# Kernel optimization log

Hardware: AMD Instinct MI355X
Metric: run time of the kernel (lower is better)

Reference implementation:

```python
import jax, jax.numpy as jnp
import numpy as np

EPS = 1e-5
NEG_SLOPE = 0.2


def knn(x, k):
    # x: (B, C, N). pairwise_distance = -||xi - xj||^2, topk -> nearest neighbors.
    xt = jnp.swapaxes(x, 1, 2)                       # (B, N, C)
    inner = -2.0 * jnp.matmul(xt, x)                 # (B, N, N)
    xx = jnp.sum(x * x, axis=1, keepdims=True)       # (B, 1, N)
    pd = -xx - inner - jnp.swapaxes(xx, 1, 2)        # (B, N, N)
    return jax.lax.top_k(pd, k)[1]                   # (B, N, k) int32


def get_graph_feature(x, k):
    # x: (B, C, N) -> (B, N, k, 2C) edge features [neighbor - center, center]
    idx = knn(x, k)
    xt = jnp.swapaxes(x, 1, 2)                       # (B, N, C)
    nb = jax.vmap(lambda f, i: f[i])(xt, idx)        # (B, N, k, C) gather
    center = xt[:, :, None, :]                       # (B, N, 1, C)
    return jnp.concatenate(
        [nb - center, jnp.broadcast_to(center, nb.shape)], axis=-1)


def edge_conv(x, w, k):
    # conv_2d with kernel 1: 1x1 conv (no bias) + InstanceNorm2d + LeakyReLU, then max over k
    feat = get_graph_feature(x, k)                   # (B, N, k, 2C)
    y = jnp.einsum('bnkc,oc->bonk', feat, w)         # (B, O, N, k)
    mean = jnp.mean(y, axis=(2, 3), keepdims=True)
    var = jnp.var(y, axis=(2, 3), keepdims=True)
    y = (y - mean) * jax.lax.rsqrt(var + EPS)        # InstanceNorm2d (no affine)
    y = jnp.where(y >= 0, y, NEG_SLOPE * y)
    return jnp.max(y, axis=-1)                       # (B, O, N)


def setup_inputs() -> dict:
    key = jax.random.key(0)
    ks = jax.random.split(key, 8)
    B, N = 16, 2048
    s = 0.05
    return {
        'x': jax.random.normal(ks[0], (B, 3, N), dtype=jnp.float32),
        'w1': jax.random.normal(ks[1], (64, 6), dtype=jnp.float32) * s,
        'w2': jax.random.normal(ks[2], (64, 128), dtype=jnp.float32) * s,
        'w3': jax.random.normal(ks[3], (128, 128), dtype=jnp.float32) * s,
        'w4': jax.random.normal(ks[4], (256, 256), dtype=jnp.float32) * s,
        'w5': jax.random.normal(ks[5], (512, 512), dtype=jnp.float32) * s,
        'bn5_gamma': jnp.ones((512,), dtype=jnp.float32),
        'bn5_beta': jnp.zeros((512,), dtype=jnp.float32),
    }


def reference(x, w1, w2, w3, w4, w5, bn5_gamma, bn5_beta):
    k = 20
    x1 = edge_conv(x, w1, k)                         # (B, 64, N)
    x2 = edge_conv(x1, w2, k)                        # (B, 64, N)
    x3 = edge_conv(x2, w3, k)                        # (B, 128, N)
    x4 = edge_conv(x3, w4, k)                        # (B, 256, N)
    x_cat = jnp.concatenate([x1, x2, x3, x4], axis=1)  # (B, 512, N)
    y = jnp.einsum('bcn,oc->bon', x_cat, w5)         # conv5, (B, 512, N)
    # BatchNorm1d (training-mode batch stats) over (B, N)
    mean = jnp.mean(y, axis=(0, 2), keepdims=True)
    var = jnp.var(y, axis=(0, 2), keepdims=True)
    y = (y - mean) * jax.lax.rsqrt(var + EPS)
    y = y * bn5_gamma[None, :, None] + bn5_beta[None, :, None]
    y = jnp.where(y >= 0, y, NEG_SLOPE * y)
    feat = jnp.concatenate([jnp.max(y, axis=2), jnp.mean(y, axis=2)], axis=1)  # (B, 1024)
    return feat
```

## Files before the change

kernel.cpp:

```cpp
#include <hip/hip_runtime.h>

#define NN 2048
#define NB 16
#define KK 20
#define EPSF 1e-5f

typedef unsigned long long ull;
typedef _Float16 v8h __attribute__((ext_vector_type(8)));
typedef float v4f __attribute__((ext_vector_type(4)));

__device__ __forceinline__ float shflx_f(float v, int m) { return __shfl_xor(v, m, 64); }
__device__ __forceinline__ ull shflx_u64(ull v, int m) {
  int lo = __shfl_xor((int)(unsigned)v, m, 64);
  int hi = __shfl_xor((int)(unsigned)(v >> 32), m, 64);
  return (((ull)(unsigned)hi) << 32) | (unsigned)lo;
}
__device__ __forceinline__ ull packkey(float s, int n) {
  unsigned u = __float_as_uint(s);
  u = (u & 0x80000000u) ? ~u : (u | 0x80000000u);
  return (((ull)u) << 32) | (unsigned)(2047 - n);
}

__global__ __launch_bounds__(256) void prep_kernel(const float* __restrict__ x,
    _Float16* __restrict__ xh, _Float16* __restrict__ xl, float* __restrict__ xx,
    int C, int KB, long bstride)
{
  const int b = blockIdx.y;
  const int n = blockIdx.x * 256 + threadIdx.x;
  const float* xb = x + (size_t)b * bstride;
  const int Cp = KB * 32;
  _Float16* ph = xh + ((size_t)b * NN + n) * Cp;
  _Float16* pl = xl + ((size_t)b * NN + n) * Cp;
  float s = 0.f;
  for (int kb = 0; kb < KB; kb++) {
    for (int g = 0; g < 4; g++) {
      v8h hv, lv;
#pragma unroll
      for (int j = 0; j < 8; j++) {
        int c = kb * 32 + g * 8 + j;
        float v = (c < C) ? xb[(size_t)c * NN + n] : 0.f;
        _Float16 h = (_Float16)v;
        hv[j] = h;
        lv[j] = (_Float16)(v - (float)h);
        s = fmaf(v, v, s);
      }
      *(v8h*)(ph + kb * 32 + g * 8) = hv;
      *(v8h*)(pl + kb * 32 + g * 8) = lv;
    }
  }
  xx[b * NN + n] = s;
}

template<int KB>
__device__ __forceinline__ void tile_scores(const v8h (&Bh)[KB], const v8h (&Bl)[KB],
    const v8h (&Ah)[4][KB], const v8h (&Al)[4][KB], float xv, v4f (&out)[4])
{
#pragma unroll
  for (int a = 0; a < 4; a++) {
    v4f a0 = {0.f, 0.f, 0.f, 0.f};
    v4f a1 = {0.f, 0.f, 0.f, 0.f};
#pragma unroll
    for (int kb = 0; kb < KB; kb++) {
      v4f& acc = (kb & 1) ? a1 : a0;
      acc = __builtin_amdgcn_mfma_f32_16x16x32_f16(Ah[a][kb], Bh[kb], acc, 0, 0, 0);
      acc = __builtin_amdgcn_mfma_f32_16x16x32_f16(Ah[a][kb], Bl[kb], acc, 0, 0, 0);
      acc = __builtin_amdgcn_mfma_f32_16x16x32_f16(Al[a][kb], Bh[kb], acc, 0, 0, 0);
    }
    v4f s = a0 + a1;
#pragma unroll
    for (int j = 0; j < 4; j++) out[a][j] = s[j] - 0.5f * xv;
  }
}

template<int KB>
__global__ __launch_bounds__(256, 1) void knn2(
    const _Float16* __restrict__ xh, const _Float16* __restrict__ xl,
    const float* __restrict__ xxg, ull* __restrict__ slistG, int* __restrict__ cntG)
{
  __shared__ float gmL[256][33];
  __shared__ float tauL[256];
  __shared__ int scnt[256];

  const int t = threadIdx.x;
  const int lane = t & 63;
  const int wave = t >> 6;
  const int col = lane & 15;
  const int quad = lane >> 4;
  const int quad8 = quad * 8;
  const int b = blockIdx.x >> 1;
  const int chunk = blockIdx.x & 1;
  const int qg = blockIdx.y;
  const int Cp = KB * 32;
  const int cb = chunk * 1024;
  const _Float16* xhb = xh + (size_t)b * NN * Cp;
  const _Float16* xlb = xl + (size_t)b * NN * Cp;
  const float* xxb = xxg + b * NN;

  v8h Ah[4][KB], Al[4][KB];
  const int qw = qg * 256 + wave * 64;
#pragma unroll
  for (int a = 0; a < 4; a++) {
    const _Float16* pa = xhb + (size_t)(qw + a * 16 + col) * Cp + quad8;
    const _Float16* pb = xlb + (size_t)(qw + a * 16 + col) * Cp + quad8;
#pragma unroll
    for (int kb = 0; kb < KB; kb++) {
      Ah[a][kb] = *(const v8h*)(pa + kb * 32);
      Al[a][kb] = *(const v8h*)(pb + kb * 32);
    }
  }

  v8h Bh[2][KB], Bl[2][KB];
  float xvb[2];
  auto loadB = [&](int slot, int tt) {
    int t2 = tt < 63 ? tt : 63;
    int n = cb + t2 * 16 + col;
    const _Float16* pb = xhb + (size_t)n * Cp + quad8;
    const _Float16* pl = xlb + (size_t)n * Cp + quad8;
#pragma unroll
    for (int kb = 0; kb < KB; kb++) {
      Bh[slot][kb] = *(const v8h*)(pb + kb * 32);
      Bl[slot][kb] = *(const v8h*)(pl + kb * 32);
    }
    xvb[slot] = xxb[n];
  };

  float gm[4][8];
#pragma unroll
  for (int a = 0; a < 4; a++)
#pragma unroll
    for (int j = 0; j < 8; j++) gm[a][j] = -3.4e38f;

  loadB(0, 0);
  for (int tt = 0; tt < 64; tt += 2) {
    loadB(1, tt + 1);
    {
      v4f out[4];
      tile_scores<KB>(Bh[0], Bl[0], Ah, Al, xvb[0], out);
#pragma unroll
      for (int a = 0; a < 4; a++)
#pragma unroll
        for (int j = 0; j < 4; j++) gm[a][j * 2] = fmaxf(gm[a][j * 2], out[a][j]);
    }
    loadB(0, tt + 2);
    {
      v4f out[4];
      tile_scores<KB>(Bh[1], Bl[1], Ah, Al, xvb[1], out);
#pragma unroll
      for (int a = 0; a < 4; a++)
#pragma unroll
        for (int j = 0; j < 4; j++) gm[a][j * 2 + 1] = fmaxf(gm[a][j * 2 + 1], out[a][j]);
    }
  }

#pragma unroll
  for (int a = 0; a < 4; a++)
#pragma unroll
    for (int j = 0; j < 4; j++) {
      int qi = wave * 64 + a * 16 + quad * 4 + j;
      gmL[qi][col * 2 + 0] = gm[a][j * 2 + 0];
      gmL[qi][col * 2 + 1] = gm[a][j * 2 + 1];
    }
  scnt[t] = 0;
  asm volatile("s_waitcnt lgkmcnt(0)" ::: "memory");

  for (int r = 0; r < 32; r++) {
    const int q = wave * 64 + r * 2 + (lane >> 5);
    const int idx = lane & 31;
    float v = gmL[q][idx];
#pragma unroll
    for (int kk = 2; kk <= 32; kk <<= 1) {
#pragma unroll
      for (int m = kk >> 1; m >= 1; m >>= 1) {
        float o = shflx_f(v, m);
        bool keepmax = ((idx & kk) == 0) == ((idx & m) == 0);
        v = keepmax ? fmaxf(v, o) : fminf(v, o);
      }
    }
    if (idx == 19) tauL[q] = v;
  }
  asm volatile("s_waitcnt lgkmcnt(0)" ::: "memory");

  float tq[4][4];
#pragma unroll
  for (int a = 0; a < 4; a++)
#pragma unroll
    for (int j = 0; j < 4; j++) tq[a][j] = tauL[wave * 64 + a * 16 + quad * 4 + j];

  ull* slB = slistG + (((size_t)b * NN + qg * 256) * 2 + chunk) * 64;
  loadB(0, 0);
  for (int tt = 0; tt < 64; tt += 2) {
    loadB(1, tt + 1);
    for (int s = 0; s < 2; s++) {
      v4f out[4];
      tile_scores<KB>(s ? Bh[1] : Bh[0], s ? Bl[1] : Bl[0], Ah, Al, xvb[s], out);
      int n = cb + (tt + s) * 16 + col;
#pragma unroll
      for (int a = 0; a < 4; a++)
#pragma unroll
        for (int j = 0; j < 4; j++) {
          float sc = out[a][j];
          if (sc >= tq[a][j]) {
            int qi = wave * 64 + a * 16 + quad * 4 + j;
            int pos = atomicAdd(&scnt[qi], 1);
            if (pos < 64) slB[(size_t)qi * 128 + pos] = packkey(sc, n);
          }
        }
      if (s == 0) loadB(0, tt + 2);
    }
  }
  asm volatile("s_waitcnt lgkmcnt(0)" ::: "memory");
  cntG[((size_t)b * NN + qg * 256 + t) * 2 + chunk] = scnt[t];
}

__global__ __launch_bounds__(256) void knn_merge(const ull* __restrict__ slistG,
    const int* __restrict__ cntG, const _Float16* __restrict__ xh,
    const _Float16* __restrict__ xl, const float* __restrict__ xxg,
    int* __restrict__ idxout, int Cp, int C)
{
  const int lane = threadIdx.x & 63, wave = threadIdx.x >> 6;
  const int b = blockIdx.y;
  const int q = blockIdx.x * 4 + wave;
  const int c0 = cntG[((size_t)b * NN + q) * 2 + 0];
  const int c1 = cntG[((size_t)b * NN + q) * 2 + 1];
  int* op = idxout + ((size_t)b * NN + q) * KK;

  if (c0 <= 64 && c1 <= 64) {
    const ull* s0 = slistG + ((size_t)b * NN + q) * 128;
    const int total = c0 + c1;
    ull e0 = 0, e1 = 0;
    int p0 = lane, p1 = lane + 64;
    if (p0 < total) e0 = (p0 < c0) ? s0[p0] : s0[64 + p0 - c0];
    if (p1 < total) e1 = (p1 < c0) ? s0[p1] : s0[64 + p1 - c0];
    for (int s = 0; s < KK; s++) {
      ull m = e0 > e1 ? e0 : e1;
      ull g = m;
#pragma unroll
      for (int d = 1; d < 64; d <<= 1) { ull o = shflx_u64(g, d); g = o > g ? o : g; }
      if (lane == 0) op[s] = 2047 - (int)(g & 0xFFFFFFFFu);
      if (e0 == g) e0 = 0; else if (e1 == g) e1 = 0;
    }
  } else {
    const _Float16* qh = xh + ((size_t)b * NN + q) * Cp;
    const _Float16* ql = xl + ((size_t)b * NN + q) * Cp;
    const float* xxb = xxg + b * NN;
    float sc[32];
#pragma unroll
    for (int i = 0; i < 32; i++) sc[i] = -0.5f * xxb[lane + 64 * i];
    for (int c = 0; c < C; c++) {
      float qv = (float)qh[c] + (float)ql[c];
      for (int i = 0; i < 32; i++) {
        int n = lane + 64 * i;
        float bv = (float)xh[((size_t)b * NN + n) * Cp + c] + (float)xl[((size_t)b * NN + n) * Cp + c];
        sc[i] = fmaf(qv, bv, sc[i]);
      }
    }
    for (int s = 0; s < KK; s++) {
      ull m = 0; int mi = -1;
      for (int i = 0; i < 32; i++) {
        ull k = packkey(sc[i], lane + 64 * i);
        if (k > m) { m = k; mi = i; }
      }
      ull g = m;
#pragma unroll
      for (int d = 1; d < 64; d <<= 1) { ull o = shflx_u64(g, d); g = o > g ? o : g; }
      if (lane == 0) op[s] = 2047 - (int)(g & 0xFFFFFFFFu);
      if (m == g && mi >= 0) sc[mi] = -3.4e38f;
    }
  }
}

__global__ __launch_bounds__(256) void wcvt_uv(const float* __restrict__ w,
    _Float16* __restrict__ wuh, _Float16* __restrict__ wul,
    _Float16* __restrict__ wvh, _Float16* __restrict__ wvl, int C, int Cp, int O)
{
  int idx = blockIdx.x * 256 + threadIdx.x;
  if (idx >= O * Cp) return;
  int o = idx / Cp, c = idx - o * Cp;
  float a = 0.f, bv = 0.f;
  if (c < C) { a = w[o * 2 * C + c]; bv = w[o * 2 * C + C + c]; }
  float v = bv - a;
  _Float16 ah = (_Float16)a; wuh[idx] = ah; wul[idx] = (_Float16)(a - (float)ah);
  _Float16 vh = (_Float16)v; wvh[idx] = vh; wvl[idx] = (_Float16)(v - (float)vh);
}

__global__ __launch_bounds__(256) void w5cvt(const float* __restrict__ w5,
    _Float16* __restrict__ w5h, _Float16* __restrict__ w5l)
{
  int idx = blockIdx.x * 256 + threadIdx.x;
  float v = w5[idx];
  _Float16 h = (_Float16)v;
  w5h[idx] = h;
  w5l[idx] = (_Float16)(v - (float)h);
}

__global__ __launch_bounds__(256) void y5cvt_kernel(const float* __restrict__ xcat,
    _Float16* __restrict__ xh, _Float16* __restrict__ xl)
{
  const int b = blockIdx.y;
  const int n = blockIdx.x * 256 + threadIdx.x;
  for (int kc = blockIdx.z * 4; kc < blockIdx.z * 4 + 4; kc++) {
    v8h h[4], l[4];
#pragma unroll
    for (int g = 0; g < 4; g++)
#pragma unroll
      for (int j = 0; j < 8; j++) {
        float v = xcat[((size_t)b * 512 + kc * 32 + g * 8 + j) * NN + n];
        _Float16 hh = (_Float16)v;
        h[g][j] = hh;
        l[g][j] = (_Float16)(v - (float)hh);
      }
    size_t base = (((size_t)b * 16 + kc) * NN + n) * 32;
#pragma unroll
    for (int g = 0; g < 4; g++) {
      *(v8h*)(xh + base + g * 8) = h[g];
      *(v8h*)(xl + base + g * 8) = l[g];
    }
  }
}

__global__ __launch_bounds__(256) void y5_mfma(const _Float16* __restrict__ w5h,
    const _Float16* __restrict__ w5l, const _Float16* __restrict__ xh,
    const _Float16* __restrict__ xl, float* __restrict__ y5)
{
  const int lane = threadIdx.x & 63, wave = threadIdx.x >> 6;
  const int col = lane & 15, quad = lane >> 4, quad8 = quad * 8;
  const int b = blockIdx.z;
  const int o0 = blockIdx.x * 256 + wave * 64;
  const int nb0 = blockIdx.y * 128;
  v4f acc[4][8];
#pragma unroll
  for (int a = 0; a < 4; a++)
#pragma unroll
    for (int t = 0; t < 8; t++) acc[a][t] = {0.f, 0.f, 0.f, 0.f};

  for (int kc = 0; kc < 16; kc++) {
    v8h Ah[4], Al[4];
#pragma unroll
    for (int a = 0; a < 4; a++) {
      size_t off = (size_t)(o0 + a * 16 + col) * 512 + kc * 32 + quad8;
      Ah[a] = *(const v8h*)(w5h + off);
      Al[a] = *(const v8h*)(w5l + off);
    }
#pragma unroll
    for (int t = 0; t < 8; t++) {
      int n = nb0 + t * 16 + col;
      size_t boff = (((size_t)b * 16 + kc) * NN + n) * 32 + quad8;
      v8h Bh = *(const v8h*)(xh + boff);
      v8h Bl = *(const v8h*)(xl + boff);
#pragma unroll
      for (int a = 0; a < 4; a++) {
        acc[a][t] = __builtin_amdgcn_mfma_f32_16x16x32_f16(Ah[a], Bh, acc[a][t], 0, 0, 0);
        acc[a][t] = __builtin_amdgcn_mfma_f32_16x16x32_f16(Ah[a], Bl, acc[a][t], 0, 0, 0);
        acc[a][t] = __builtin_amdgcn_mfma_f32_16x16x32_f16(Al[a], Bh, acc[a][t], 0, 0, 0);
      }
    }
  }
#pragma unroll
  for (int a = 0; a < 4; a++)
#pragma unroll
    for (int t = 0; t < 8; t++)
#pragma unroll
      for (int j = 0; j < 4; j++)
        y5[((size_t)b * 512 + o0 + a * 16 + quad * 4 + j) * NN + nb0 + t * 16 + col] = acc[a][t][j];
}

__global__ __launch_bounds__(256) void uv_mfma(const _Float16* __restrict__ wuh,
    const _Float16* __restrict__ wul, const _Float16* __restrict__ wvh,
    const _Float16* __restrict__ wvl, const _Float16* __restrict__ xh,
    const _Float16* __restrict__ xl, float* __restrict__ Uc, float* __restrict__ Vc,
    int Cp)
{
  const int lane = threadIdx.x & 63, wave = threadIdx.x >> 6;
  const int col = lane & 15, quad = lane >> 4, quad8 = quad * 8;
  const int b = blockIdx.z;
  const int o0 = blockIdx.x * 32;
  const int nb0 = blockIdx.y * 512 + wave * 128;
  v4f aU[2][8], aV[2][8];
#pragma unroll
  for (int a = 0; a < 2; a++)
#pragma unroll
    for (int t = 0; t < 8; t++) { aU[a][t] = {0.f,0.f,0.f,0.f}; aV[a][t] = {0.f,0.f,0.f,0.f}; }

  const int KBr = Cp >> 5;
  for (int kb = 0; kb < KBr; kb++) {
    v8h Uh[2], Ul[2], Vh[2], Vl[2];
#pragma unroll
    for (int a = 0; a < 2; a++) {
      size_t off = (size_t)(o0 + a * 16 + col) * Cp + kb * 32 + quad8;
      Uh[a] = *(const v8h*)(wuh + off);
      Ul[a] = *(const v8h*)(wul + off);
      Vh[a] = *(const v8h*)(wvh + off);
      Vl[a] = *(const v8h*)(wvl + off);
    }
#pragma unroll
    for (int t = 0; t < 8; t++) {
      int n = nb0 + t * 16 + col;
      size_t boff = ((size_t)b * NN + n) * Cp + kb * 32 + quad8;
      v8h Bh = *(const v8h*)(xh + boff);
      v8h Bl = *(const v8h*)(xl + boff);
#pragma unroll
      for (int a = 0; a < 2; a++) {
        aU[a][t] = __builtin_amdgcn_mfma_f32_16x16x32_f16(Uh[a], Bh, aU[a][t], 0, 0, 0);
        aU[a][t] = __builtin_amdgcn_mfma_f32_16x16x32_f16(Uh[a], Bl, aU[a][t], 0, 0, 0);
        aU[a][t] = __builtin_amdgcn_mfma_f32_16x16x32_f16(Ul[a], Bh, aU[a][t], 0, 0, 0);
        aV[a][t] = __builtin_amdgcn_mfma_f32_16x16x32_f16(Vh[a], Bh, aV[a][t], 0, 0, 0);
        aV[a][t] = __builtin_amdgcn_mfma_f32_16x16x32_f16(Vh[a], Bl, aV[a][t], 0, 0, 0);
        aV[a][t] = __builtin_amdgcn_mfma_f32_16x16x32_f16(Vl[a], Bh, aV[a][t], 0, 0, 0);
      }
    }
  }
#pragma unroll
  for (int a = 0; a < 2; a++)
#pragma unroll
    for (int t = 0; t < 8; t++)
#pragma unroll
      for (int j = 0; j < 4; j++) {
        size_t base = ((size_t)b * 64 + o0 + a * 16 + quad * 4 + j) * NN + nb0 + t * 16 + col;
        Uc[base] = aU[a][t][j];
        Vc[base] = aV[a][t][j];
      }
}

__global__ __launch_bounds__(256) void edge_kernel(const float* __restrict__ Uc,
    const float* __restrict__ Vc, const int* __restrict__ idx,
    float* __restrict__ xo)
{
  __shared__ float Ur[4 * 2052];
  __shared__ float red[8][4];
  __shared__ float smv[8];
  const int b = blockIdx.y, o0 = blockIdx.x * 4;
  const int t = threadIdx.x, lane = t & 63, wave = t >> 6;
  for (int r = 0; r < 4; r++)
    for (int i = t; i < NN; i += 256)
      Ur[r * 2052 + i] = Uc[((size_t)b * 64 + o0 + r) * NN + i];
  __syncthreads();
  const float* Vb = Vc + ((size_t)b * 64 + o0) * NN;
  const int* ib = idx + (size_t)b * NN * KK;
  float s0 = 0, s1 = 0, s2 = 0, s3 = 0, c0 = 0, c1 = 0, c2 = 0, c3 = 0;
  for (int n = t; n < NN; n += 256) {
    float v0 = Vb[n], v1 = Vb[NN + n], v2 = Vb[2 * NN + n], v3 = Vb[3 * NN + n];
    const int* ip = ib + (size_t)n * KK;
#pragma unroll
    for (int j = 0; j < KK; j++) {
      int m = ip[j];
      float y0 = Ur[m] + v0, y1 = Ur[2052 + m] + v1;
      float y2 = Ur[4104 + m] + v2, y3 = Ur[6156 + m] + v3;
      s0 += y0; c0 = fmaf(y0, y0, c0);
      s1 += y1; c1 = fmaf(y1, y1, c1);
      s2 += y2; c2 = fmaf(y2, y2, c2);
      s3 += y3; c3 = fmaf(y3, y3, c3);
    }
  }
  float sa[4] = { s0, s1, s2, s3 }, ca[4] = { c0, c1, c2, c3 };
#pragma unroll
  for (int r = 0; r < 4; r++) {
    float a = sa[r], c = ca[r];
#pragma unroll
    for (int d = 1; d < 64; d <<= 1) { a += shflx_f(a, d); c += shflx_f(c, d); }
    if (lane == 0) { red[r][wave] = a; red[4 + r][wave] = c; }
  }
  __syncthreads();
  if (t < 4) {
    float a = red[t][0] + red[t][1] + red[t][2] + red[t][3];
    float c = red[4 + t][0] + red[4 + t][1] + red[4 + t][2] + red[4 + t][3];
    const float inv = 1.f / (float)(NN * KK);
    float mu = a * inv;
    float var = fmaxf(c * inv - mu * mu, 0.f);
    smv[t] = mu;
    smv[4 + t] = rsqrtf(var + EPSF);
  }
  __syncthreads();
  const float mu0 = smv[0], mu1 = smv[1], mu2 = smv[2], mu3 = smv[3];
  const float i0 = smv[4], i1 = smv[5], i2 = smv[6], i3 = smv[7];
  for (int n = t; n < NN; n += 256) {
    float v0 = Vb[n], v1 = Vb[NN + n], v2 = Vb[2 * NN + n], v3 = Vb[3 * NN + n];
    const int* ip = ib + (size_t)n * KK;
    float m0 = -3.4e38f, m1 = m0, m2 = m0, m3 = m0;
#pragma unroll
    for (int j = 0; j < KK; j++) {
      int m = ip[j];
      m0 = fmaxf(m0, Ur[m] + v0);
      m1 = fmaxf(m1, Ur[2052 + m] + v1);
      m2 = fmaxf(m2, Ur[4104 + m] + v2);
      m3 = fmaxf(m3, Ur[6156 + m] + v3);
    }
    float z;
    z = (m0 - mu0) * i0; xo[((size_t)b * 512 + o0 + 0) * NN + n] = z >= 0.f ? z : 0.2f * z;
    z = (m1 - mu1) * i1; xo[((size_t)b * 512 + o0 + 1) * NN + n] = z >= 0.f ? z : 0.2f * z;
    z = (m2 - mu2) * i2; xo[((size_t)b * 512 + o0 + 2) * NN + n] = z >= 0.f ? z : 0.2f * z;
    z = (m3 - mu3) * i3; xo[((size_t)b * 512 + o0 + 3) * NN + n] = z >= 0.f ? z : 0.2f * z;
  }
}

__global__ __launch_bounds__(256) void bn5stat_kernel(const float* __restrict__ y5,
    float* __restrict__ bn5) {
  __shared__ float rs[4], rq[4];
  const int o = blockIdx.x, t = threadIdx.x, lane = t & 63, wave = t >> 6;
  float s = 0.f, q = 0.f;
  for (int b = 0; b < NB; b++) {
    const float* p = y5 + ((size_t)b * 512 + o) * NN;
    for (int n = t; n < NN; n += 256) { float v = p[n]; s += v; q = fmaf(v, v, q); }
  }
#pragma unroll
  for (int d = 1; d < 64; d <<= 1) { s += shflx_f(s, d); q += shflx_f(q, d); }
  if (lane == 0) { rs[wave] = s; rq[wave] = q; }
  __syncthreads();
  if (t == 0) {
    float S = rs[0] + rs[1] + rs[2] + rs[3];
    float Q = rq[0] + rq[1] + rq[2] + rq[3];
    const float inv = 1.f / (float)(NB * NN);
    float mu = S * inv;
    float var = fmaxf(Q * inv - mu * mu, 0.f);
    bn5[o] = mu;
    bn5[512 + o] = rsqrtf(var + EPSF);
  }
}

__global__ __launch_bounds__(256) void final_kernel(const float* __restrict__ y5,
    const float* __restrict__ bn5, const float* __restrict__ gamma,
    const float* __restrict__ beta, float* __restrict__ out)
{
  __shared__ float rm[4], rs[4];
  const int o = blockIdx.x, b = blockIdx.y, t = threadIdx.x, lane = t & 63, wave = t >> 6;
  const float mu = bn5[o], iv = bn5[512 + o], g = gamma[o], be = beta[o];
  const float* p = y5 + ((size_t)b * 512 + o) * NN;
  float mx = -3.4e38f, sm = 0.f;
  for (int n = t; n < NN; n += 256) {
    float z = (p[n] - mu) * iv;
    z = z * g + be;
    z = (z >= 0.f) ? z : 0.2f * z;
    mx = fmaxf(mx, z);
    sm += z;
  }
#pragma unroll
  for (int d = 1; d < 64; d <<= 1) { mx = fmaxf(mx, shflx_f(mx, d)); sm += shflx_f(sm, d); }
  if (lane == 0) { rm[wave] = mx; rs[wave] = sm; }
  __syncthreads();
  if (t == 0) {
    float M = fmaxf(fmaxf(rm[0], rm[1]), fmaxf(rm[2], rm[3]));
    float S = rs[0] + rs[1] + rs[2] + rs[3];
    out[(size_t)b * 1024 + o] = M;
    out[(size_t)b * 1024 + 512 + o] = S * (1.f / NN);
  }
}

extern "C" void kernel_launch(void* const* d_in, const int* in_sizes, int n_in,
                              void* d_out, int out_size, void* d_ws, size_t ws_size,
                              hipStream_t stream)
{
  (void)in_sizes; (void)n_in; (void)out_size; (void)ws_size;
  const float* x  = (const float*)d_in[0];
  const float* w1 = (const float*)d_in[1];
  const float* w2 = (const float*)d_in[2];
  const float* w3 = (const float*)d_in[3];
  const float* w4 = (const float*)d_in[4];
  const float* w5 = (const float*)d_in[5];
  const float* g5 = (const float*)d_in[6];
  const float* b5 = (const float*)d_in[7];
  float* out = (float*)d_out;

  float* ws   = (float*)d_ws;
  float* xcat = ws;
  float* Ub   = xcat + 16777216;
  float* Vb   = Ub + 8388608;
  int*   idxb = (int*)(Vb + 8388608);
  float* xxb  = (float*)(idxb + 655360);
  float* bn5  = xxb + 32768;

  _Float16* xth = (_Float16*)Vb;
  _Float16* xtl = xth + (size_t)NB * NN * 128;
  int* cntb = (int*)(Vb + 4194304);
  float* Vc = Vb + 4259840;
  _Float16* wuh = (_Float16*)(Vb + 6356992);
  _Float16* wul = wuh + 32768;
  _Float16* wvh = wul + 32768;
  _Float16* wvl = wvh + 32768;

  ull* slist = (ull*)Ub;
  float* Uc = Ub;

  _Float16* w5h = (_Float16*)idxb;
  _Float16* w5l = w5h + 262144;
  _Float16* xcfh = (_Float16*)Ub;
  _Float16* xcfl = (_Float16*)Vb;
  float* y5 = xcat;

  struct Lyr { const float* xin; long bstride; int C, KB, O, coff; const float* w; };
  const Lyr L[4] = {
    { x,              3L * NN,   3,   1, 64,  0,   w1 },
    { xcat,           512L * NN, 64,  2, 64,  64,  w2 },
    { xcat + 64 * NN, 512L * NN, 64,  2, 128, 128, w3 },
    { xcat + 128 * NN,512L * NN, 128, 4, 256, 256, w4 },
  };

  for (int l = 0; l < 4; l++) {
    const int Cp = L[l].KB * 32, O = L[l].O;
    prep_kernel<<<dim3(NN / 256, NB), 256, 0, stream>>>(L[l].xin, xth, xtl, xxb,
                                                        L[l].C, L[l].KB, L[l].bstride);
    switch (L[l].KB) {
      case 1: knn2<1><<<dim3(NB * 2, NN / 256), 256, 0, stream>>>(xth, xtl, xxb, slist, cntb); break;
      case 2: knn2<2><<<dim3(NB * 2, NN / 256), 256, 0, stream>>>(xth, xtl, xxb, slist, cntb); break;
      default: knn2<4><<<dim3(NB * 2, NN / 256), 256, 0, stream>>>(xth, xtl, xxb, slist, cntb); break;
    }
    knn_merge<<<dim3(NN / 4, NB), 256, 0, stream>>>(slist, cntb, xth, xtl, xxb, idxb,
                                                    Cp, L[l].C);
    wcvt_uv<<<(O * Cp + 255) / 256, 256, 0, stream>>>(L[l].w, wuh, wul, wvh, wvl,
                                                      L[l].C, Cp, O);
    for (int c0 = 0; c0 < O; c0 += 64) {
      uv_mfma<<<dim3(2, NN / 512, NB), 256, 0, stream>>>(
          wuh + (size_t)c0 * Cp, wul + (size_t)c0 * Cp,
          wvh + (size_t)c0 * Cp, wvl + (size_t)c0 * Cp,
          xth, xtl, Uc, Vc, Cp);
      edge_kernel<<<dim3(16, NB), 256, 0, stream>>>(Uc, Vc, idxb,
          xcat + (size_t)(L[l].coff + c0) * NN);
    }
  }
  w5cvt<<<1024, 256, 0, stream>>>(w5, w5h, w5l);
  y5cvt_kernel<<<dim3(NN / 256, NB, 4), 256, 0, stream>>>(xcat, xcfh, xcfl);
  y5_mfma<<<dim3(2, NN / 128, NB), 256, 0, stream>>>(w5h, w5l, xcfh, xcfl, y5);
  bn5stat_kernel<<<512, 256, 0, stream>>>(y5, bn5);
  final_kernel<<<dim3(512, NB), 256, 0, stream>>>(y5, bn5, g5, b5, out);
}
```

Baseline: 1.743 ms.

## Fuse edge-conv outputs into next-layer fp16 inputs and compute instance-norm stats algebraically

The edge kernel now gathers U once per point, keeping the max and sum over neighbours. The instance-norm statistics are rebuilt from those sums, a neighbour-count histogram and V moments, so the second gather pass is gone. It writes the split-fp16 layouts for the next layer's kNN and for the conv5 GEMM directly, and accumulates squared norms with atomics. This removes the per-layer prep kernel, the xcat fp32 buffer and the y5 conversion pass. The kNN B-tile prefetch is deepened from 2 to 4 slots, and uv_mfma now covers larger output chunks per launch. In exchange the norm maths is more complex, relies on atomics, and adds register pressure.

Measured after the change: 2.566 ms. +47.2%, slower.

```diff
diff --git a/kernel.cpp b/kernel.cpp
--- a/kernel.cpp
+++ b/kernel.cpp
@@ -7,6 +7,7 @@
 
 typedef unsigned long long ull;
 typedef _Float16 v8h __attribute__((ext_vector_type(8)));
+typedef _Float16 v4h __attribute__((ext_vector_type(4)));
 typedef float v4f __attribute__((ext_vector_type(4)));
 
 __device__ __forceinline__ float shflx_f(float v, int m) { return __shfl_xor(v, m, 64); }
@@ -109,8 +110,8 @@
     }
   }
 
-  v8h Bh[2][KB], Bl[2][KB];
-  float xvb[2];
+  v8h Bh[4][KB], Bl[4][KB];
+  float xvb[4];
   auto loadB = [&](int slot, int tt) {
     int t2 = tt < 63 ? tt : 63;
     int n = cb + t2 * 16 + col;
@@ -130,25 +131,19 @@
 #pragma unroll
     for (int j = 0; j < 8; j++) gm[a][j] = -3.4e38f;
 
-  loadB(0, 0);
-  for (int tt = 0; tt < 64; tt += 2) {
-    loadB(1, tt + 1);
-    {
+#pragma unroll
+  for (int s = 0; s < 4; s++) loadB(s, s);
+  for (int tt = 0; tt < 64; tt += 4) {
+#pragma unroll
+    for (int s = 0; s < 4; s++) {
       v4f out[4];
-      tile_scores<KB>(Bh[0], Bl[0], Ah, Al, xvb[0], out);
+      tile_scores<KB>(Bh[s], Bl[s], Ah, Al, xvb[s], out);
+      loadB(s, tt + 4 + s);
+      const int par = s & 1;
 #pragma unroll
       for (int a = 0; a < 4; a++)
 #pragma unroll
-        for (int j = 0; j < 4; j++) gm[a][j * 2] = fmaxf(gm[a][j * 2], out[a][j]);
-    }
-    loadB(0, tt + 2);
-    {
-      v4f out[4];
-      tile_scores<KB>(Bh[1], Bl[1], Ah, Al, xvb[1], out);
-#pragma unroll
-      for (int a = 0; a < 4; a++)
-#pragma unroll
-        for (int j = 0; j < 4; j++) gm[a][j * 2 + 1] = fmaxf(gm[a][j * 2 + 1], out[a][j]);
+        for (int j = 0; j < 4; j++) gm[a][j * 2 + par] = fmaxf(gm[a][j * 2 + par], out[a][j]);
     }
   }
 
@@ -187,12 +182,14 @@
     for (int j = 0; j < 4; j++) tq[a][j] = tauL[wave * 64 + a * 16 + quad * 4 + j];
 
   ull* slB = slistG + (((size_t)b * NN + qg * 256) * 2 + chunk) * 64;
-  loadB(0, 0);
-  for (int tt = 0; tt < 64; tt += 2) {
-    loadB(1, tt + 1);
-    for (int s = 0; s < 2; s++) {
+#pragma unroll
+  for (int s = 0; s < 4; s++) loadB(s, s);
+  for (int tt = 0; tt < 64; tt += 4) {
+#pragma unroll
+    for (int s = 0; s < 4; s++) {
       v4f out[4];
-      tile_scores<KB>(s ? Bh[1] : Bh[0], s ? Bl[1] : Bl[0], Ah, Al, xvb[s], out);
+      tile_scores<KB>(Bh[s], Bl[s], Ah, Al, xvb[s], out);
+      loadB(s, tt + 4 + s);
       int n = cb + (tt + s) * 16 + col;
 #pragma unroll
       for (int a = 0; a < 4; a++)
@@ -205,7 +202,6 @@
             if (pos < 64) slB[(size_t)qi * 128 + pos] = packkey(sc, n);
           }
         }
-      if (s == 0) loadB(0, tt + 2);
     }
   }
   asm volatile("s_waitcnt lgkmcnt(0)" ::: "memory");
@@ -269,18 +265,34 @@
   }
 }
 
-__global__ __launch_bounds__(256) void wcvt_uv(const float* __restrict__ w,
+__global__ __launch_bounds__(256) void setup_kernel(const int* __restrict__ idx,
+    int* __restrict__ cnt, const float* __restrict__ w,
     _Float16* __restrict__ wuh, _Float16* __restrict__ wul,
-    _Float16* __restrict__ wvh, _Float16* __restrict__ wvl, int C, int Cp, int O)
-{
-  int idx = blockIdx.x * 256 + threadIdx.x;
-  if (idx >= O * Cp) return;
-  int o = idx / Cp, c = idx - o * Cp;
-  float a = 0.f, bv = 0.f;
-  if (c < C) { a = w[o * 2 * C + c]; bv = w[o * 2 * C + C + c]; }
-  float v = bv - a;
-  _Float16 ah = (_Float16)a; wuh[idx] = ah; wul[idx] = (_Float16)(a - (float)ah);
-  _Float16 vh = (_Float16)v; wvh[idx] = vh; wvl[idx] = (_Float16)(v - (float)vh);
+    _Float16* __restrict__ wvh, _Float16* __restrict__ wvl,
+    int C, int Cp, int O, float* __restrict__ xx, int zxx)
+{
+  __shared__ int h[2048];
+  const int blk = blockIdx.x, t = threadIdx.x;
+  if (blk < NB) {
+    const int b = blk;
+    for (int i = t; i < 2048; i += 256) h[i] = 0;
+    if (zxx) for (int i = t; i < 2048; i += 256) xx[b * 2048 + i] = 0.f;
+    __syncthreads();
+    const int* ib = idx + (size_t)b * NN * KK;
+    for (int i = t; i < NN * KK; i += 256) atomicAdd(&h[ib[i]], 1);
+    __syncthreads();
+    for (int i = t; i < 2048; i += 256) cnt[b * 2048 + i] = h[i];
+  } else {
+    int e = (blk - NB) * 256 + t;
+    if (e < O * Cp) {
+      int o = e / Cp, c = e - o * Cp;
+      float a = 0.f, bv = 0.f;
+      if (c < C) { a = w[o * 2 * C + c]; bv = w[o * 2 * C + C + c]; }
+      float v = bv - a;
+      _Float16 ah = (_Float16)a; wuh[e] = ah; wul[e] = (_Float16)(a - (float)ah);
+      _Float16 vh = (_Float16)v; wvh[e] = vh; wvl[e] = (_Float16)(v - (float)vh);
+    }
+  }
 }
 
 __global__ __launch_bounds__(256) void w5cvt(const float* __restrict__ w5,
@@ -293,82 +305,11 @@
   w5l[idx] = (_Float16)(v - (float)h);
 }
 
-__global__ __launch_bounds__(256) void y5cvt_kernel(const float* __restrict__ xcat,
-    _Float16* __restrict__ xh, _Float16* __restrict__ xl)
-{
-  const int b = blockIdx.y;
-  const int n = blockIdx.x * 256 + threadIdx.x;
-  for (int kc = blockIdx.z * 4; kc < blockIdx.z * 4 + 4; kc++) {
-    v8h h[4], l[4];
-#pragma unroll
-    for (int g = 0; g < 4; g++)
-#pragma unroll
-      for (int j = 0; j < 8; j++) {
-        float v = xcat[((size_t)b * 512 + kc * 32 + g * 8 + j) * NN + n];
-        _Float16 hh = (_Float16)v;
-        h[g][j] = hh;
-        l[g][j] = (_Float16)(v - (float)hh);
-      }
-    size_t base = (((size_t)b * 16 + kc) * NN + n) * 32;
-#pragma unroll
-    for (int g = 0; g < 4; g++) {
-      *(v8h*)(xh + base + g * 8) = h[g];
-      *(v8h*)(xl + base + g * 8) = l[g];
-    }
-  }
-}
-
-__global__ __launch_bounds__(256) void y5_mfma(const _Float16* __restrict__ w5h,
-    const _Float16* __restrict__ w5l, const _Float16* __restrict__ xh,
-    const _Float16* __restrict__ xl, float* __restrict__ y5)
-{
-  const int lane = threadIdx.x & 63, wave = threadIdx.x >> 6;
-  const int col = lane & 15, quad = lane >> 4, quad8 = quad * 8;
-  const int b = blockIdx.z;
-  const int o0 = blockIdx.x * 256 + wave * 64;
-  const int nb0 = blockIdx.y * 128;
-  v4f acc[4][8];
-#pragma unroll
-  for (int a = 0; a < 4; a++)
-#pragma unroll
-    for (int t = 0; t < 8; t++) acc[a][t] = {0.f, 0.f, 0.f, 0.f};
-
-  for (int kc = 0; kc < 16; kc++) {
-    v8h Ah[4], Al[4];
-#pragma unroll
-    for (int a = 0; a < 4; a++) {
-      size_t off = (size_t)(o0 + a * 16 + col) * 512 + kc * 32 + quad8;
-      Ah[a] = *(const v8h*)(w5h + off);
-      Al[a] = *(const v8h*)(w5l + off);
-    }
-#pragma unroll
-    for (int t = 0; t < 8; t++) {
-      int n = nb0 + t * 16 + col;
-      size_t boff = (((size_t)b * 16 + kc) * NN + n) * 32 + quad8;
-      v8h Bh = *(const v8h*)(xh + boff);
-      v8h Bl = *(const v8h*)(xl + boff);
-#pragma unroll
-      for (int a = 0; a < 4; a++) {
-        acc[a][t] = __builtin_amdgcn_mfma_f32_16x16x32_f16(Ah[a], Bh, acc[a][t], 0, 0, 0);
-        acc[a][t] = __builtin_amdgcn_mfma_f32_16x16x32_f16(Ah[a], Bl, acc[a][t], 0, 0, 0);
-        acc[a][t] = __builtin_amdgcn_mfma_f32_16x16x32_f16(Al[a], Bh, acc[a][t], 0, 0, 0);
-      }
-    }
-  }
-#pragma unroll
-  for (int a = 0; a < 4; a++)
-#pragma unroll
-    for (int t = 0; t < 8; t++)
-#pragma unroll
-      for (int j = 0; j < 4; j++)
-        y5[((size_t)b * 512 + o0 + a * 16 + quad * 4 + j) * NN + nb0 + t * 16 + col] = acc[a][t][j];
-}
-
 __global__ __launch_bounds__(256) void uv_mfma(const _Float16* __restrict__ wuh,
     const _Float16* __restrict__ wul, const _Float16* __restrict__ wvh,
     const _Float16* __restrict__ wvl, const _Float16* __restrict__ xh,
-    const _Float16* __restrict__ xl, float* __restrict__ Uc, float* __restrict__ Vc,
-    int Cp)
+    const _Float16* __restrict__ xl, float* __restrict__ Uo, float* __restrict__ Vo,
+    int Cp, int Och)
 {
   const int lane = threadIdx.x & 63, wave = threadIdx.x >> 6;
   const int col = lane & 15, quad = lane >> 4, quad8 = quad * 8;
@@ -415,81 +356,166 @@
     for (int t = 0; t < 8; t++)
 #pragma unroll
       for (int j = 0; j < 4; j++) {
-        size_t base = ((size_t)b * 64 + o0 + a * 16 + quad * 4 + j) * NN + nb0 + t * 16 + col;
-        Uc[base] = aU[a][t][j];
-        Vc[base] = aV[a][t][j];
+        size_t base = ((size_t)b * Och + o0 + a * 16 + quad * 4 + j) * NN + nb0 + t * 16 + col;
+        Uo[base] = aU[a][t][j];
+        Vo[base] = aV[a][t][j];
       }
 }
 
-__global__ __launch_bounds__(256) void edge_kernel(const float* __restrict__ Uc,
-    const float* __restrict__ Vc, const int* __restrict__ idx,
-    float* __restrict__ xo)
+__global__ __launch_bounds__(256) void edge2(const float* __restrict__ U,
+    const float* __restrict__ V, const int* __restrict__ idx,
+    const int* __restrict__ cnt,
+    _Float16* __restrict__ nxh, _Float16* __restrict__ nxl, int CpN,
+    _Float16* __restrict__ y5h, _Float16* __restrict__ y5l, int gbase,
+    float* __restrict__ xx, int Och)
 {
   __shared__ float Ur[4 * 2052];
-  __shared__ float red[8][4];
+  __shared__ float red[20][4];
   __shared__ float smv[8];
   const int b = blockIdx.y, o0 = blockIdx.x * 4;
   const int t = threadIdx.x, lane = t & 63, wave = t >> 6;
   for (int r = 0; r < 4; r++)
     for (int i = t; i < NN; i += 256)
-      Ur[r * 2052 + i] = Uc[((size_t)b * 64 + o0 + r) * NN + i];
+      Ur[r * 2052 + i] = U[((size_t)b * Och + o0 + r) * NN + i];
   __syncthreads();
-  const float* Vb = Vc + ((size_t)b * 64 + o0) * NN;
+  const float* Vp = V + ((size_t)b * Och + o0) * NN;
   const int* ib = idx + (size_t)b * NN * KK;
-  float s0 = 0, s1 = 0, s2 = 0, s3 = 0, c0 = 0, c1 = 0, c2 = 0, c3 = 0;
-  for (int n = t; n < NN; n += 256) {
-    float v0 = Vb[n], v1 = Vb[NN + n], v2 = Vb[2 * NN + n], v3 = Vb[3 * NN + n];
+  const int* cb = cnt + b * NN;
+
+  float sG[4] = {0,0,0,0}, sVG[4] = {0,0,0,0}, sV[4] = {0,0,0,0},
+        sV2[4] = {0,0,0,0}, sU2[4] = {0,0,0,0};
+  float Mr[4][8], Vr[4][8];
+#pragma unroll
+  for (int ni = 0; ni < 8; ni++) {
+    const int n = t + ni * 256;
     const int* ip = ib + (size_t)n * KK;
+    float G0 = 0, G1 = 0, G2 = 0, G3 = 0;
+    float M0 = -3.4e38f, M1 = M0, M2 = M0, M3 = M0;
 #pragma unroll
     for (int j = 0; j < KK; j++) {
       int m = ip[j];
-      float y0 = Ur[m] + v0, y1 = Ur[2052 + m] + v1;
-      float y2 = Ur[4104 + m] + v2, y3 = Ur[6156 + m] + v3;
-      s0 += y0; c0 = fmaf(y0, y0, c0);
-      s1 += y1; c1 = fmaf(y1, y1, c1);
-      s2 += y2; c2 = fmaf(y2, y2, c2);
-      s3 += y3; c3 = fmaf(y3, y3, c3);
-    }
-  }
-  float sa[4] = { s0, s1, s2, s3 }, ca[4] = { c0, c1, c2, c3 };
+      float u0 = Ur[m], u1 = Ur[2052 + m], u2 = Ur[4104 + m], u3 = Ur[6156 + m];
+      G0 += u0; M0 = fmaxf(M0, u0);
+      G1 += u1; M1 = fmaxf(M1, u1);
+      G2 += u2; M2 = fmaxf(M2, u2);
+      G3 += u3; M3 = fmaxf(M3, u3);
+    }
+    float v0 = Vp[n], v1 = Vp[NN + n], v2 = Vp[2 * NN + n], v3 = Vp[3 * NN + n];
+    sG[0] += G0; sVG[0] = fmaf(v0, G0, sVG[0]); sV[0] += v0; sV2[0] = fmaf(v0, v0, sV2[0]);
+    sG[1] += G1; sVG[1] = fmaf(v1, G1, sVG[1]); sV[1] += v1; sV2[1] = fmaf(v1, v1, sV2[1]);
+    sG[2] += G2; sVG[2] = fmaf(v2, G2, sVG[2]); sV[2] += v2; sV2[2] = fmaf(v2, v2, sV2[2]);
+    sG[3] += G3; sVG[3] = fmaf(v3, G3, sVG[3]); sV[3] += v3; sV2[3] = fmaf(v3, v3, sV2[3]);
+    Mr[0][ni] = M0; Mr[1][ni] = M1; Mr[2][ni] = M2; Mr[3][ni] = M3;
+    Vr[0][ni] = v0; Vr[1][ni] = v1; Vr[2][ni] = v2; Vr[3][ni] = v3;
+  }
+  for (int i = t; i < NN; i += 256) {
+    float c = (float)cb[i];
+    float u0 = Ur[i], u1 = Ur[2052 + i], u2 = Ur[4104 + i], u3 = Ur[6156 + i];
+    sU2[0] = fmaf(c * u0, u0, sU2[0]);
+    sU2[1] = fmaf(c * u1, u1, sU2[1]);
+    sU2[2] = fmaf(c * u2, u2, sU2[2]);
+    sU2[3] = fmaf(c * u3, u3, sU2[3]);
+  }
+  float st[20];
 #pragma unroll
   for (int r = 0; r < 4; r++) {
-    float a = sa[r], c = ca[r];
-#pragma unroll
-    for (int d = 1; d < 64; d <<= 1) { a += shflx_f(a, d); c += shflx_f(c, d); }
-    if (lane == 0) { red[r][wave] = a; red[4 + r][wave] = c; }
+    st[r] = sG[r]; st[4 + r] = sVG[r]; st[8 + r] = sV[r];
+    st[12 + r] = sV2[r]; st[16 + r] = sU2[r];
+  }
+#pragma unroll
+  for (int k = 0; k < 20; k++) {
+    float a = st[k];
+#pragma unroll
+    for (int d = 1; d < 64; d <<= 1) a += shflx_f(a, d);
+    if (lane == 0) red[k][wave] = a;
   }
   __syncthreads();
   if (t < 4) {
-    float a = red[t][0] + red[t][1] + red[t][2] + red[t][3];
-    float c = red[4 + t][0] + red[4 + t][1] + red[4 + t][2] + red[4 + t][3];
+    float g  = red[t][0] + red[t][1] + red[t][2] + red[t][3];
+    float vg = red[4 + t][0] + red[4 + t][1] + red[4 + t][2] + red[4 + t][3];
+    float v  = red[8 + t][0] + red[8 + t][1] + red[8 + t][2] + red[8 + t][3];
+    float v2 = red[12 + t][0] + red[12 + t][1] + red[12 + t][2] + red[12 + t][3];
+    float u2 = red[16 + t][0] + red[16 + t][1] + red[16 + t][2] + red[16 + t][3];
+    float sumY  = g + (float)KK * v;
+    float sumY2 = u2 + 2.f * vg + (float)KK * v2;
     const float inv = 1.f / (float)(NN * KK);
-    float mu = a * inv;
-    float var = fmaxf(c * inv - mu * mu, 0.f);
+    float mu = sumY * inv;
+    float var = fmaxf(sumY2 * inv - mu * mu, 0.f);
     smv[t] = mu;
     smv[4 + t] = rsqrtf(var + EPSF);
   }
   __syncthreads();
   const float mu0 = smv[0], mu1 = smv[1], mu2 = smv[2], mu3 = smv[3];
   const float i0 = smv[4], i1 = smv[5], i2 = smv[6], i3 = smv[7];
-  for (int n = t; n < NN; n += 256) {
-    float v0 = Vb[n], v1 = Vb[NN + n], v2 = Vb[2 * NN + n], v3 = Vb[3 * NN + n];
-    const int* ip = ib + (size_t)n * KK;
-    float m0 = -3.4e38f, m1 = m0, m2 = m0, m3 = m0;
-#pragma unroll
-    for (int j = 0; j < KK; j++) {
-      int m = ip[j];
-      m0 = fmaxf(m0, Ur[m] + v0);
-      m1 = fmaxf(m1, Ur[2052 + m] + v1);
-      m2 = fmaxf(m2, Ur[4104 + m] + v2);
-      m3 = fmaxf(m3, Ur[6156 + m] + v3);
-    }
-    float z;
-    z = (m0 - mu0) * i0; xo[((size_t)b * 512 + o0 + 0) * NN + n] = z >= 0.f ? z : 0.2f * z;
-    z = (m1 - mu1) * i1; xo[((size_t)b * 512 + o0 + 1) * NN + n] = z >= 0.f ? z : 0.2f * z;
-    z = (m2 - mu2) * i2; xo[((size_t)b * 512 + o0 + 2) * NN + n] = z >= 0.f ? z : 0.2f * z;
-    z = (m3 - mu3) * i3; xo[((size_t)b * 512 + o0 + 3) * NN + n] = z >= 0.f ? z : 0.2f * z;
-  }
+  const int kc = (gbase + o0) >> 5, c32 = (gbase + o0) & 31;
+#pragma unroll
+  for (int ni = 0; ni < 8; ni++) {
+    const int n = t + ni * 256;
+    float z0 = (Mr[0][ni] + Vr[0][ni] - mu0) * i0; z0 = z0 >= 0.f ? z0 : 0.2f * z0;
+    float z1 = (Mr[1][ni] + Vr[1][ni] - mu1) * i1; z1 = z1 >= 0.f ? z1 : 0.2f * z1;
+    float z2 = (Mr[2][ni] + Vr[2][ni] - mu2) * i2; z2 = z2 >= 0.f ? z2 : 0.2f * z2;
+    float z3 = (Mr[3][ni] + Vr[3][ni] - mu3) * i3; z3 = z3 >= 0.f ? z3 : 0.2f * z3;
+    v4h h4, l4;
+    h4[0] = (_Float16)z0; l4[0] = (_Float16)(z0 - (float)h4[0]);
+    h4[1] = (_Float16)z1; l4[1] = (_Float16)(z1 - (float)h4[1]);
+    h4[2] = (_Float16)z2; l4[2] = (_Float16)(z2 - (float)h4[2]);
+    h4[3] = (_Float16)z3; l4[3] = (_Float16)(z3 - (float)h4[3]);
+    size_t yoff = (((size_t)b * 16 + kc) * NN + n) * 32 + c32;
+    *(v4h*)(y5h + yoff) = h4;
+    *(v4h*)(y5l + yoff) = l4;
+    if (nxh) {
+      size_t noff = ((size_t)b * NN + n) * CpN + o0;
+      *(v4h*)(nxh + noff) = h4;
+      *(v4h*)(nxl + noff) = l4;
+      atomicAdd(&xx[b * NN + n], z0 * z0 + z1 * z1 + z2 * z2 + z3 * z3);
+    }
+  }
+}
+
+__global__ __launch_bounds__(256) void y5_mfma(const _Float16* __restrict__ w5h,
+    const _Float16* __restrict__ w5l, const _Float16* __restrict__ xh,
+    const _Float16* __restrict__ xl, float* __restrict__ y5)
+{
+  const int lane = threadIdx.x & 63, wave = threadIdx.x >> 6;
+  const int col = lane & 15, quad = lane >> 4, quad8 = quad * 8;
+  const int b = blockIdx.z;
+  const int o0 = blockIdx.x * 256 + wave * 64;
+  const int nb0 = blockIdx.y * 128;
+  v4f acc[4][8];
+#pragma unroll
+  for (int a = 0; a < 4; a++)
+#pragma unroll
+    for (int t = 0; t < 8; t++) acc[a][t] = {0.f, 0.f, 0.f, 0.f};
+
+  for (int kc = 0; kc < 16; kc++) {
+    v8h Ah[4], Al[4];
+#pragma unroll
+    for (int a = 0; a < 4; a++) {
+      size_t off = (size_t)(o0 + a * 16 + col) * 512 + kc * 32 + quad8;
+      Ah[a] = *(const v8h*)(w5h + off);
+      Al[a] = *(const v8h*)(w5l + off);
+    }
+#pragma unroll
+    for (int t = 0; t < 8; t++) {
+      int n = nb0 + t * 16 + col;
+      size_t boff = (((size_t)b * 16 + kc) * NN + n) * 32 + quad8;
+      v8h Bh = *(const v8h*)(xh + boff);
+      v8h Bl = *(const v8h*)(xl + boff);
+#pragma unroll
+      for (int a = 0; a < 4; a++) {
+        acc[a][t] = __builtin_amdgcn_mfma_f32_16x16x32_f16(Ah[a], Bh, acc[a][t], 0, 0, 0);
+        acc[a][t] = __builtin_amdgcn_mfma_f32_16x16x32_f16(Ah[a], Bl, acc[a][t], 0, 0, 0);
+        acc[a][t] = __builtin_amdgcn_mfma_f32_16x16x32_f16(Al[a], Bh, acc[a][t], 0, 0, 0);
+      }
+    }
+  }
+#pragma unroll
+  for (int a = 0; a < 4; a++)
+#pragma unroll
+    for (int t = 0; t < 8; t++)
+#pragma unroll
+      for (int j = 0; j < 4; j++)
+        y5[((size_t)b * 512 + o0 + a * 16 + quad * 4 + j) * NN + nb0 + t * 16 + col] = acc[a][t][j];
 }
 
 __global__ __launch_bounds__(256) void bn5stat_kernel(const float* __restrict__ y5,
@@ -560,64 +586,67 @@
   float* out = (float*)d_out;
 
   float* ws   = (float*)d_ws;
-  float* xcat = ws;
-  float* Ub   = xcat + 16777216;
+  _Float16* y5fh = (_Float16*)ws;
+  _Float16* y5fl = y5fh + 16777216;
+  float* Ub   = ws + 16777216;
   float* Vb   = Ub + 8388608;
   int*   idxb = (int*)(Vb + 8388608);
   float* xxb  = (float*)(idxb + 655360);
   float* bn5  = xxb + 32768;
 
   _Float16* xth = (_Float16*)Vb;
-  _Float16* xtl = xth + (size_t)NB * NN * 128;
+  _Float16* xtl = xth + 4194304;
   int* cntb = (int*)(Vb + 4194304);
-  float* Vc = Vb + 4259840;
-  _Float16* wuh = (_Float16*)(Vb + 6356992);
+  int* cnth = (int*)(Vb + 4259840);
+  _Float16* wuh = (_Float16*)(Vb + 4292608);
   _Float16* wul = wuh + 32768;
   _Float16* wvh = wul + 32768;
   _Float16* wvl = wvh + 32768;
 
   ull* slist = (ull*)Ub;
-  float* Uc = Ub;
+  float* Uo = Ub;
+  float* Vo = Ub + 4194304;
+  float* y5 = Ub;
 
   _Float16* w5h = (_Float16*)idxb;
   _Float16* w5l = w5h + 262144;
-  _Float16* xcfh = (_Float16*)Ub;
-  _Float16* xcfl = (_Float16*)Vb;
-  float* y5 = xcat;
-
-  struct Lyr { const float* xin; long bstride; int C, KB, O, coff; const float* w; };
+
+  struct Lyr { int C, KB, O, coff, CpN; const float* w; };
   const Lyr L[4] = {
-    { x,              3L * NN,   3,   1, 64,  0,   w1 },
-    { xcat,           512L * NN, 64,  2, 64,  64,  w2 },
-    { xcat + 64 * NN, 512L * NN, 64,  2, 128, 128, w3 },
-    { xcat + 128 * NN,512L * NN, 128, 4, 256, 256, w4 },
+    { 3,   1, 64,  0,   64,  w1 },
+    { 64,  2, 64,  64,  64,  w2 },
+    { 64,  2, 128, 128, 128, w3 },
+    { 128, 4, 256, 256, 0,   w4 },
   };
 
+  prep_kernel<<<dim3(NN / 256, NB), 256, 0, stream>>>(x, xth, xtl, xxb, 3, 1, 3L * NN);
+
   for (int l = 0; l < 4; l++) {
-    const int Cp = L[l].KB * 32, O = L[l].O;
-    prep_kernel<<<dim3(NN / 256, NB), 256, 0, stream>>>(L[l].xin, xth, xtl, xxb,
-                                                        L[l].C, L[l].KB, L[l].bstride);
+    const int Cp = L[l].KB * 32, O = L[l].O, C = L[l].C;
     switch (L[l].KB) {
       case 1: knn2<1><<<dim3(NB * 2, NN / 256), 256, 0, stream>>>(xth, xtl, xxb, slist, cntb); break;
       case 2: knn2<2><<<dim3(NB * 2, NN / 256), 256, 0, stream>>>(xth, xtl, xxb, slist, cntb); break;
       default: knn2<4><<<dim3(NB * 2, NN / 256), 256, 0, stream>>>(xth, xtl, xxb, slist, cntb); break;
     }
-    knn_merge<<<dim3(NN / 4, NB), 256, 0, stream>>>(slist, cntb, xth, xtl, xxb, idxb,
-                                                    Cp, L[l].C);
-    wcvt_uv<<<(O * Cp + 255) / 256, 256, 0, stream>>>(L[l].w, wuh, wul, wvh, wvl,
-                                                      L[l].C, Cp, O);
-    for (int c0 = 0; c0 < O; c0 += 64) {
-      uv_mfma<<<dim3(2, NN / 512, NB), 256, 0, stream>>>(
+    knn_merge<<<dim3(NN / 4, NB), 256, 0, stream>>>(slist, cntb, xth, xtl, xxb, idxb, Cp, C);
+    const int wblocks = (O * Cp + 255) / 256;
+    setup_kernel<<<NB + wblocks, 256, 0, stream>>>(idxb, cnth, L[l].w,
+        wuh, wul, wvh, wvl, C, Cp, O, xxb, l < 3 ? 1 : 0);
+    const int nchunks = (O > 128) ? 2 : 1;
+    const int Och = O / nchunks;
+    for (int c = 0; c < nchunks; c++) {
+      const int c0 = c * Och;
+      uv_mfma<<<dim3(Och / 32, NN / 512, NB), 256, 0, stream>>>(
           wuh + (size_t)c0 * Cp, wul + (size_t)c0 * Cp,
           wvh + (size_t)c0 * Cp, wvl + (size_t)c0 * Cp,
-          xth, xtl, Uc, Vc, Cp);
-      edge_kernel<<<dim3(16, NB), 256, 0, stream>>>(Uc, Vc, idxb,
-          xcat + (size_t)(L[l].coff + c0) * NN);
+          xth, xtl, Uo, Vo, Cp, Och);
+      edge2<<<dim3(Och / 4, NB), 256, 0, stream>>>(Uo, Vo, idxb, cnth,
+          (l < 3) ? xth : (_Float16*)nullptr, (l < 3) ? xtl : (_Float16*)nullptr,
+          L[l].CpN, y5fh, y5fl, L[l].coff + c0, xxb, Och);
     }
   }
   w5cvt<<<1024, 256, 0, stream>>>(w5, w5h, w5l);
-  y5cvt_kernel<<<dim3(NN / 256, NB, 4), 256, 0, stream>>>(xcat, xcfh, xcfl);
-  y5_mfma<<<dim3(2, NN / 128, NB), 256, 0, stream>>>(w5h, w5l, xcfh, xcfl, y5);
+  y5_mfma<<<dim3(2, NN / 128, NB), 256, 0, stream>>>(w5h, w5l, y5fh, y5fl, y5);
   bn5stat_kernel<<<512, 256, 0, stream>>>(y5, bn5);
   final_kernel<<<dim3(512, NB), 256, 0, stream>>>(y5, bn5, g5, b5, out);
 }
```
